# Kernel optimization log

Measured on AMD Instinct MI355X. Metric: run time of the kernel, lower is better.

## Reference

```python
import jax, jax.numpy as jnp
import numpy as np

OUT_FEATURES = 4096
IN_FEATURES = 16384
NNZ = 2_000_000
BATCH = 128


def setup_inputs() -> dict:
    key = jax.random.key(0)
    k1, k2, k3, k4, k5 = jax.random.split(key, 5)
    inputs = jax.random.normal(k1, (BATCH, IN_FEATURES), dtype=jnp.float32)
    # learned sparse weight values and bias (uniform init like reset_parameters)
    bound = 1.0 / (IN_FEATURES ** 0.5)
    values = jax.random.uniform(k2, (NNZ,), minval=-bound, maxval=bound, dtype=jnp.float32)
    bias = jax.random.uniform(k3, (OUT_FEATURES,), minval=-bound, maxval=bound, dtype=jnp.float32)
    # fixed COO connectivity: rows -> out_features, cols -> in_features
    rows = jax.random.randint(k4, (NNZ,), 0, OUT_FEATURES, dtype=jnp.int32)
    cols = jax.random.randint(k5, (NNZ,), 0, IN_FEATURES, dtype=jnp.int32)
    return {"inputs": inputs, "values": values, "bias": bias, "rows": rows, "cols": cols}


def reference(inputs, values, bias, rows, cols):
    # out[b, r] = sum_{k: rows[k]==r} values[k] * inputs[b, cols[k]]  (+ bias[r])
    # Gather input columns per nnz entry, scale, then scatter-add into output rows.
    contrib = inputs[:, cols] * values            # [B, nnz]
    out = jax.ops.segment_sum(contrib.T, rows, num_segments=OUT_FEATURES).T  # [B, out_features]
    return out + bias
```

## Files before the change

kernel.cpp:

```cpp
#include <hip/hip_runtime.h>
#include <hip/hip_fp16.h>

#define NNZ    2000000
#define BATCH  128
#define IN_F   16384
#define OUT_F  4096
#define NCH    512
#define CHUNK  ((NNZ + NCH - 1) / NCH)
#define NBK    1024
#define RPB    4
#define BK_CAP 2320

__device__ inline int mbcnt64(unsigned long long m) {
  return __builtin_amdgcn_mbcnt_hi((unsigned)(m >> 32),
         __builtin_amdgcn_mbcnt_lo((unsigned)m, 0));
}

__global__ __launch_bounds__(512)
void k_localsort(const int* __restrict__ rows, const int* __restrict__ cols,
                 const float* __restrict__ vals, int* __restrict__ desc,
                 int2* __restrict__ pairs) {
  __shared__ int  lrows[CHUNK];
  __shared__ int2 stage[CHUNK];
  __shared__ int  h[NBK], cur[NBK];
  __shared__ int  wsums[8];
  const int t = threadIdx.x, c = blockIdx.x;
  const int lane = t & 63, w = t >> 6;
  const int base = c * CHUNK;
  const int n = min(CHUNK, NNZ - base);

  h[t] = 0; h[t + 512] = 0;
  __syncthreads();
  for (int i = t; i < n; i += 512) {
    const int r = rows[base + i];
    lrows[i] = r;
    atomicAdd(&h[r >> 2], 1);
  }
  __syncthreads();
  const int v0 = h[2 * t], v1 = h[2 * t + 1];
  const int sv = v0 + v1;
  int x = sv;
#pragma unroll
  for (int off = 1; off < 64; off <<= 1) { int y = __shfl_up(x, off); if (lane >= off) x += y; }
  if (lane == 63) wsums[w] = x;
  __syncthreads();
  int wex = 0;
#pragma unroll
  for (int j = 0; j < 8; ++j) { const int sj = wsums[j]; wex += (j < w) ? sj : 0; }
  const int excl = wex + x - sv;
  cur[2 * t] = excl;
  cur[2 * t + 1] = excl + v0;
  ((int2*)desc)[c * 512 + t] = make_int2((excl << 8) | v0, ((excl + v0) << 8) | v1);
  __syncthreads();
  for (int i = t; i < n; i += 512) {
    const int r = lrows[i];
    const int pos = atomicAdd(&cur[r >> 2], 1);
    stage[pos] = make_int2((r << 14) | cols[base + i], __float_as_int(vals[base + i]));
  }
  __syncthreads();
  for (int j = t; j < n; j += 512) pairs[base + j] = stage[j];
}

__global__ __launch_bounds__(512)
void k_cscan(const int* __restrict__ desc, unsigned* __restrict__ rdesc,
             int* __restrict__ btot) {
  __shared__ int tile[16 * 513];
  const int t = threadIdx.x, blk = blockIdx.x;
  const int b0 = blk * 16;
  const int lane = t & 63, w = t >> 6;
#pragma unroll
  for (int it = 0; it < 16; ++it) {
    const int c = it * 32 + (t >> 4);
    tile[(t & 15) * 513 + c] = desc[c * NBK + b0 + (t & 15)];
  }
  __syncthreads();
#pragma unroll
  for (int k = 0; k < 2; ++k) {
    const int bl = 2 * w + k;
    int carry = 0;
#pragma unroll
    for (int j = 0; j < 8; ++j) {
      const int c = j * 64 + lane;
      const unsigned d = (unsigned)tile[bl * 513 + c];
      const int len = (int)(d & 255u);
      int x = len;
#pragma unroll
      for (int off = 1; off < 64; off <<= 1) { int y = __shfl_up(x, off); if (lane >= off) x += y; }
      const int ex = carry + x - len;
      rdesc[(b0 + bl) * NCH + c] = (d << 12) | (unsigned)ex;
      carry += __shfl(x, 63);
    }
    if (lane == 0) btot[b0 + bl] = carry;
  }
}

__global__ __launch_bounds__(256)
void k_transpose(const float* __restrict__ in, __half* __restrict__ inT) {
  __shared__ float tile[32][33];
  const int tx = threadIdx.x, ty = threadIdx.y;
  const int c0 = blockIdx.x * 32, b0 = blockIdx.y * 32;
#pragma unroll
  for (int j = 0; j < 32; j += 8)
    tile[ty + j][tx] = in[(b0 + ty + j) * IN_F + c0 + tx];
  __syncthreads();
#pragma unroll
  for (int j = 0; j < 32; j += 8)
    inT[(size_t)(c0 + ty + j) * BATCH + b0 + tx] = __float2half(tile[tx][ty + j]);
}

#define FMA8(V, X) do { \
    const __half2* hh = (const __half2*)&(X); \
    float2 f0 = __half22float2(hh[0]); \
    float2 f1 = __half22float2(hh[1]); \
    float2 f2 = __half22float2(hh[2]); \
    float2 f3 = __half22float2(hh[3]); \
    a0 = fmaf((V), f0.x, a0); a1 = fmaf((V), f0.y, a1); \
    a2 = fmaf((V), f1.x, a2); a3 = fmaf((V), f1.y, a3); \
    a4 = fmaf((V), f2.x, a4); a5 = fmaf((V), f2.y, a5); \
    a6 = fmaf((V), f3.x, a6); a7 = fmaf((V), f3.y, a7); \
  } while (0)

#define REFILL(SL, KK) do { \
    const int idx = (hh_ + 2 * (KK)) * 8 + 2 * g; \
    const int i0_ = (idx < nr) ? (s + idx) : 0; \
    const int i1_ = (idx + 1 < nr) ? (s + idx + 1) : 0; \
    const int2 p0 = sorted[i0_]; \
    const int2 p1 = sorted[i1_]; \
    v##SL##0 = (idx < nr) ? __int_as_float(p0.y) : 0.f; \
    v##SL##1 = (idx + 1 < nr) ? __int_as_float(p1.y) : 0.f; \
    x##SL##0 = inT[(p0.x & 16383) * 16 + q]; \
    x##SL##1 = inT[(p1.x & 16383) * 16 + q]; \
  } while (0)

#define STAGE(SL, NEXTKK) do { \
    FMA8(v##SL##0, x##SL##0); \
    FMA8(v##SL##1, x##SL##1); \
    REFILL(SL, NEXTKK); \
  } while (0)

__global__ __launch_bounds__(512, 8)
void k_spmm(const uint4* __restrict__ inT, const int2* __restrict__ pairs,
            const unsigned* __restrict__ rdesc, const int* __restrict__ btot,
            const float* __restrict__ bias, float* __restrict__ out) {
  __shared__ int2 staging[BK_CAP];
  __shared__ int2 sorted[BK_CAP];
  __shared__ int  exd[NCH];
  __shared__ float part[RPB][BATCH];
  __shared__ int  wrun[32];
  __shared__ unsigned long long wmask[32];
  __shared__ int  wcnt[32];
  __shared__ int  lst[RPB + 1];
  const int t = threadIdx.x, b = blockIdx.x;
  const int w = t >> 6, lane = t & 63;
  const int n = min(btot[b], BK_CAP);
  const int nrnd = (n + 511) & ~511;

  exd[t] = (int)rdesc[b * NCH + t];
  __syncthreads();
  for (int i = t; i < n; i += 512) {
    int lo = 0, hi = NCH - 1;
#pragma unroll
    for (int st = 0; st < 9; ++st) {
      const int mid = (lo + hi + 1) >> 1;
      if ((exd[mid] & 4095) <= i) lo = mid; else hi = mid - 1;
    }
    const unsigned d = (unsigned)exd[lo];
    staging[i] = pairs[lo * CHUNK + (int)(d >> 20) + (i - (int)(d & 4095u))];
  }
  __syncthreads();

  int cnt = 0;
  for (int i = w * 64 + lane; i < nrnd; i += 512) {
    const bool valid = i < n;
    const int key = valid ? staging[i].x : 0;
    const int r4 = valid ? ((key >> 14) & 3) : 4;
    unsigned long long m[4];
#pragma unroll
    for (int r = 0; r < 4; ++r) m[r] = __ballot(r4 == r);
    if (lane < 4) cnt += __popcll(m[lane]);
  }
  if (lane < 4) wcnt[w * 4 + lane] = cnt;
  __syncthreads();

  if (w == 0 && lane < 32) {
    const int v = wcnt[lane];
    int x = v;
#pragma unroll
    for (int off = 4; off < 32; off <<= 1) { int y = __shfl_up(x, off); if (lane >= off) x += y; }
    const int exw = x - v;
    int lstr = 0;
#pragma unroll
    for (int rr = 0; rr < 4; ++rr) {
      const int tr = __shfl(x, 28 + rr);
      if ((lane & 3) > rr) lstr += tr;
    }
    wrun[lane] = lstr + exw;
    if (lane < 4) lst[lane] = lstr;
    if (lane == 0) lst[RPB] = n;
  }
  __syncthreads();

  for (int i = w * 64 + lane; i < nrnd; i += 512) {
    const bool valid = i < n;
    const int2 p = valid ? staging[i] : make_int2(0, 0);
    const int r4 = valid ? ((p.x >> 14) & 3) : 4;
    unsigned long long m[4];
#pragma unroll
    for (int r = 0; r < 4; ++r) m[r] = __ballot(r4 == r);
    if (lane < 4) wmask[w * 4 + lane] = m[lane];
    if (valid) {
      const int rank = wrun[w * 4 + r4] + mbcnt64(wmask[w * 4 + r4]);
      sorted[rank] = p;
    }
    if (lane < 4) wrun[w * 4 + lane] += __popcll(m[lane]);
  }
  __syncthreads();

  const int rloc = w >> 1, hh_ = w & 1;
  const int r = b * RPB + rloc;
  const int g = lane >> 4, q = lane & 15;
  const int s = lst[rloc];
  const int nr = lst[rloc + 1] - s;
  const int nsteps = (nr + 7) >> 3;
  const int K = (nsteps + 1) >> 1;
  const int K3 = ((K + 2) / 3) * 3;

  float a0 = 0.f, a1 = 0.f, a2 = 0.f, a3 = 0.f, a4 = 0.f, a5 = 0.f, a6 = 0.f, a7 = 0.f;
  uint4 xA0, xA1, xB0, xB1, xC0, xC1;
  float vA0, vA1, vB0, vB1, vC0, vC1;

  REFILL(A, 0);
  REFILL(B, 1);
  REFILL(C, 2);
  for (int kk = 0; kk < K3; kk += 3) {
    STAGE(A, kk + 3);
    STAGE(B, kk + 4);
    STAGE(C, kk + 5);
  }

  a0 += __shfl_xor(a0, 16); a0 += __shfl_xor(a0, 32);
  a1 += __shfl_xor(a1, 16); a1 += __shfl_xor(a1, 32);
  a2 += __shfl_xor(a2, 16); a2 += __shfl_xor(a2, 32);
  a3 += __shfl_xor(a3, 16); a3 += __shfl_xor(a3, 32);
  a4 += __shfl_xor(a4, 16); a4 += __shfl_xor(a4, 32);
  a5 += __shfl_xor(a5, 16); a5 += __shfl_xor(a5, 32);
  a6 += __shfl_xor(a6, 16); a6 += __shfl_xor(a6, 32);
  a7 += __shfl_xor(a7, 16); a7 += __shfl_xor(a7, 32);

  if (hh_ == 1 && g == 0) {
    const int o = q * 8;
    part[rloc][o + 0] = a0; part[rloc][o + 1] = a1;
    part[rloc][o + 2] = a2; part[rloc][o + 3] = a3;
    part[rloc][o + 4] = a4; part[rloc][o + 5] = a5;
    part[rloc][o + 6] = a6; part[rloc][o + 7] = a7;
  }
  __syncthreads();
  if (hh_ == 0 && g == 0) {
    const float bs_ = bias[r];
    const int o = q * 8;
    out[(o + 0) * OUT_F + r] = a0 + part[rloc][o + 0] + bs_;
    out[(o + 1) * OUT_F + r] = a1 + part[rloc][o + 1] + bs_;
    out[(o + 2) * OUT_F + r] = a2 + part[rloc][o + 2] + bs_;
    out[(o + 3) * OUT_F + r] = a3 + part[rloc][o + 3] + bs_;
    out[(o + 4) * OUT_F + r] = a4 + part[rloc][o + 4] + bs_;
    out[(o + 5) * OUT_F + r] = a5 + part[rloc][o + 5] + bs_;
    out[(o + 6) * OUT_F + r] = a6 + part[rloc][o + 6] + bs_;
    out[(o + 7) * OUT_F + r] = a7 + part[rloc][o + 7] + bs_;
  }
}

extern "C" void kernel_launch(void* const* d_in, const int* in_sizes, int n_in,
                              void* d_out, int out_size, void* d_ws, size_t ws_size,
                              hipStream_t stream) {
  const float* inputs = (const float*)d_in[0];
  const float* values = (const float*)d_in[1];
  const float* bias   = (const float*)d_in[2];
  const int*   rows   = (const int*)d_in[3];
  const int*   cols   = (const int*)d_in[4];
  float* out = (float*)d_out;

  char* ws = (char*)d_ws;
  __half*   inputT = (__half*)(ws);
  int2*     pairs  = (int2*)(ws + 4194304);
  int*      desc   = (int*)(ws + 20194304);
  unsigned* rdesc  = (unsigned*)(ws + 22291456);
  int*      btot   = (int*)(ws + 24388608);

  k_localsort<<<NCH,      512, 0, stream>>>(rows, cols, values, desc, pairs);
  k_cscan    <<<NBK / 16, 512, 0, stream>>>(desc, rdesc, btot);
  k_transpose<<<dim3(IN_F / 32, BATCH / 32), dim3(32, 8), 0, stream>>>(inputs, inputT);
  k_spmm     <<<NBK,      512, 0, stream>>>((const uint4*)inputT, pairs, rdesc, btot, bias, out);
}
```

Measured before the change: 139.4 us.

## Use packed fp16 FMA accumulation, paired nnz loads, and finer local-sort chunks

The SpMM inner loop now accumulates with packed half2 FMAs into fp16 partial sums, flushed into fp32 accumulators every three stages. This replaces per-element half-to-float conversions and scalar fp32 FMAs. Each row segment in the sorted list is padded to even length so two nnz entries can be fetched with one 16-byte LDS load. The local sort uses 1024 chunks with int4/float4 vectorized loads and int4 stores, the column scan is retuned to match, and the reduction buffer reuses the staging shared memory to cut LDS footprint. Accumulating in fp16 reduces precision of the partial sums.

Result: faster. 133.2 us (-4.4%).

```diff
diff --git a/kernel.cpp b/kernel.cpp
--- a/kernel.cpp
+++ b/kernel.cpp
@@ -5,11 +5,11 @@
 #define BATCH  128
 #define IN_F   16384
 #define OUT_F  4096
-#define NCH    512
-#define CHUNK  ((NNZ + NCH - 1) / NCH)
+#define NCH    1024
+#define CHUNK  1956
 #define NBK    1024
 #define RPB    4
-#define BK_CAP 2320
+#define BK_CAP 2240
 
 __device__ inline int mbcnt64(unsigned long long m) {
   return __builtin_amdgcn_mbcnt_hi((unsigned)(m >> 32),
@@ -28,13 +28,17 @@
   const int lane = t & 63, w = t >> 6;
   const int base = c * CHUNK;
   const int n = min(CHUNK, NNZ - base);
+  const int n4 = n >> 2;
 
   h[t] = 0; h[t + 512] = 0;
   __syncthreads();
-  for (int i = t; i < n; i += 512) {
-    const int r = rows[base + i];
-    lrows[i] = r;
-    atomicAdd(&h[r >> 2], 1);
+  for (int i = t; i < n4; i += 512) {
+    const int4 r4 = ((const int4*)(rows + base))[i];
+    ((int4*)lrows)[i] = r4;
+    atomicAdd(&h[r4.x >> 2], 1);
+    atomicAdd(&h[r4.y >> 2], 1);
+    atomicAdd(&h[r4.z >> 2], 1);
+    atomicAdd(&h[r4.w >> 2], 1);
   }
   __syncthreads();
   const int v0 = h[2 * t], v1 = h[2 * t + 1];
@@ -52,46 +56,49 @@
   cur[2 * t + 1] = excl + v0;
   ((int2*)desc)[c * 512 + t] = make_int2((excl << 8) | v0, ((excl + v0) << 8) | v1);
   __syncthreads();
-  for (int i = t; i < n; i += 512) {
-    const int r = lrows[i];
-    const int pos = atomicAdd(&cur[r >> 2], 1);
-    stage[pos] = make_int2((r << 14) | cols[base + i], __float_as_int(vals[base + i]));
-  }
-  __syncthreads();
-  for (int j = t; j < n; j += 512) pairs[base + j] = stage[j];
+  for (int i = t; i < n4; i += 512) {
+    const int4   r4 = ((const int4*)lrows)[i];
+    const int4   c4 = ((const int4*)(cols + base))[i];
+    const float4 f4 = ((const float4*)(vals + base))[i];
+    int pos;
+    pos = atomicAdd(&cur[r4.x >> 2], 1); stage[pos] = make_int2((r4.x << 14) | c4.x, __float_as_int(f4.x));
+    pos = atomicAdd(&cur[r4.y >> 2], 1); stage[pos] = make_int2((r4.y << 14) | c4.y, __float_as_int(f4.y));
+    pos = atomicAdd(&cur[r4.z >> 2], 1); stage[pos] = make_int2((r4.z << 14) | c4.z, __float_as_int(f4.z));
+    pos = atomicAdd(&cur[r4.w >> 2], 1); stage[pos] = make_int2((r4.w << 14) | c4.w, __float_as_int(f4.w));
+  }
+  __syncthreads();
+  const int nh = n >> 1;
+  for (int j = t; j < nh; j += 512)
+    ((int4*)(pairs + base))[j] = ((const int4*)stage)[j];
 }
 
 __global__ __launch_bounds__(512)
 void k_cscan(const int* __restrict__ desc, unsigned* __restrict__ rdesc,
              int* __restrict__ btot) {
-  __shared__ int tile[16 * 513];
+  __shared__ int tile[8 * 1025];
   const int t = threadIdx.x, blk = blockIdx.x;
-  const int b0 = blk * 16;
+  const int b0 = blk * 8;
   const int lane = t & 63, w = t >> 6;
 #pragma unroll
   for (int it = 0; it < 16; ++it) {
-    const int c = it * 32 + (t >> 4);
-    tile[(t & 15) * 513 + c] = desc[c * NBK + b0 + (t & 15)];
-  }
-  __syncthreads();
-#pragma unroll
-  for (int k = 0; k < 2; ++k) {
-    const int bl = 2 * w + k;
-    int carry = 0;
-#pragma unroll
-    for (int j = 0; j < 8; ++j) {
-      const int c = j * 64 + lane;
-      const unsigned d = (unsigned)tile[bl * 513 + c];
-      const int len = (int)(d & 255u);
-      int x = len;
-#pragma unroll
-      for (int off = 1; off < 64; off <<= 1) { int y = __shfl_up(x, off); if (lane >= off) x += y; }
-      const int ex = carry + x - len;
-      rdesc[(b0 + bl) * NCH + c] = (d << 12) | (unsigned)ex;
-      carry += __shfl(x, 63);
-    }
-    if (lane == 0) btot[b0 + bl] = carry;
-  }
+    const int cc = it * 64 + (t >> 3);
+    tile[(t & 7) * 1025 + cc] = desc[cc * NBK + b0 + (t & 7)];
+  }
+  __syncthreads();
+  int carry = 0;
+#pragma unroll
+  for (int j = 0; j < 16; ++j) {
+    const int cc = j * 64 + lane;
+    const unsigned d = (unsigned)tile[w * 1025 + cc];
+    const int len = (int)(d & 255u);
+    int x = len;
+#pragma unroll
+    for (int off = 1; off < 64; off <<= 1) { int y = __shfl_up(x, off); if (lane >= off) x += y; }
+    const int ex = carry + x - len;
+    rdesc[(b0 + w) * NCH + cc] = (d << 12) | (unsigned)ex;
+    carry += __shfl(x, 63);
+  }
+  if (lane == 0) btot[b0 + w] = carry;
 }
 
 __global__ __launch_bounds__(256)
@@ -108,44 +115,45 @@
     inT[(size_t)(c0 + ty + j) * BATCH + b0 + tx] = __float2half(tile[tx][ty + j]);
 }
 
-#define FMA8(V, X) do { \
-    const __half2* hh = (const __half2*)&(X); \
-    float2 f0 = __half22float2(hh[0]); \
-    float2 f1 = __half22float2(hh[1]); \
-    float2 f2 = __half22float2(hh[2]); \
-    float2 f3 = __half22float2(hh[3]); \
-    a0 = fmaf((V), f0.x, a0); a1 = fmaf((V), f0.y, a1); \
-    a2 = fmaf((V), f1.x, a2); a3 = fmaf((V), f1.y, a3); \
-    a4 = fmaf((V), f2.x, a4); a5 = fmaf((V), f2.y, a5); \
-    a6 = fmaf((V), f3.x, a6); a7 = fmaf((V), f3.y, a7); \
-  } while (0)
-
 #define REFILL(SL, KK) do { \
     const int idx = (hh_ + 2 * (KK)) * 8 + 2 * g; \
-    const int i0_ = (idx < nr) ? (s + idx) : 0; \
-    const int i1_ = (idx + 1 < nr) ? (s + idx + 1) : 0; \
-    const int2 p0 = sorted[i0_]; \
-    const int2 p1 = sorted[i1_]; \
-    v##SL##0 = (idx < nr) ? __int_as_float(p0.y) : 0.f; \
-    v##SL##1 = (idx + 1 < nr) ? __int_as_float(p1.y) : 0.f; \
-    x##SL##0 = inT[(p0.x & 16383) * 16 + q]; \
-    x##SL##1 = inT[(p1.x & 16383) * 16 + q]; \
+    const bool vld = idx < nr; \
+    const int i0_ = vld ? (s + idx) : 0; \
+    uint4 pp = *((const uint4*)(sorted + i0_)); \
+    if (!vld) { pp.y = 0u; pp.w = 0u; } \
+    x##SL##0 = inT[(pp.x & 16383u) * 16 + q]; \
+    x##SL##1 = inT[(pp.z & 16383u) * 16 + q]; \
+    pv##SL = make_uint2(pp.y, pp.w); \
   } while (0)
 
-#define STAGE(SL, NEXTKK) do { \
-    FMA8(v##SL##0, x##SL##0); \
-    FMA8(v##SL##1, x##SL##1); \
-    REFILL(SL, NEXTKK); \
+#define FMAH(SL) do { \
+    const __half2 hv0 = __float2half2_rn(__uint_as_float(pv##SL.x)); \
+    const __half2 hv1 = __float2half2_rn(__uint_as_float(pv##SL.y)); \
+    const __half2* h0 = (const __half2*)&x##SL##0; \
+    const __half2* h1 = (const __half2*)&x##SL##1; \
+    hac0 = __hfma2(hv0, h0[0], hac0); hac1 = __hfma2(hv0, h0[1], hac1); \
+    hac2 = __hfma2(hv0, h0[2], hac2); hac3 = __hfma2(hv0, h0[3], hac3); \
+    hac0 = __hfma2(hv1, h1[0], hac0); hac1 = __hfma2(hv1, h1[1], hac1); \
+    hac2 = __hfma2(hv1, h1[2], hac2); hac3 = __hfma2(hv1, h1[3], hac3); \
+  } while (0)
+
+#define STAGE(SL, NEXTKK) do { FMAH(SL); REFILL(SL, NEXTKK); } while (0)
+
+#define FLUSH() do { \
+    float2 f0 = __half22float2(hac0), f1 = __half22float2(hac1); \
+    float2 f2 = __half22float2(hac2), f3 = __half22float2(hac3); \
+    a0 += f0.x; a1 += f0.y; a2 += f1.x; a3 += f1.y; \
+    a4 += f2.x; a5 += f2.y; a6 += f3.x; a7 += f3.y; \
+    hac0 = hz; hac1 = hz; hac2 = hz; hac3 = hz; \
   } while (0)
 
 __global__ __launch_bounds__(512, 8)
 void k_spmm(const uint4* __restrict__ inT, const int2* __restrict__ pairs,
             const unsigned* __restrict__ rdesc, const int* __restrict__ btot,
             const float* __restrict__ bias, float* __restrict__ out) {
-  __shared__ int2 staging[BK_CAP];
-  __shared__ int2 sorted[BK_CAP];
+  __shared__ __align__(16) int2 staging[BK_CAP];
+  __shared__ __align__(16) int2 sorted[BK_CAP + 8];
   __shared__ int  exd[NCH];
-  __shared__ float part[RPB][BATCH];
   __shared__ int  wrun[32];
   __shared__ unsigned long long wmask[32];
   __shared__ int  wcnt[32];
@@ -156,11 +164,12 @@
   const int nrnd = (n + 511) & ~511;
 
   exd[t] = (int)rdesc[b * NCH + t];
+  exd[t + 512] = (int)rdesc[b * NCH + t + 512];
   __syncthreads();
   for (int i = t; i < n; i += 512) {
     int lo = 0, hi = NCH - 1;
 #pragma unroll
-    for (int st = 0; st < 9; ++st) {
+    for (int st = 0; st < 10; ++st) {
       const int mid = (lo + hi + 1) >> 1;
       if ((exd[mid] & 4095) <= i) lo = mid; else hi = mid - 1;
     }
@@ -188,15 +197,20 @@
 #pragma unroll
     for (int off = 4; off < 32; off <<= 1) { int y = __shfl_up(x, off); if (lane >= off) x += y; }
     const int exw = x - v;
-    int lstr = 0;
+    int lstr = 0, tpad = 0;
 #pragma unroll
     for (int rr = 0; rr < 4; ++rr) {
       const int tr = __shfl(x, 28 + rr);
-      if ((lane & 3) > rr) lstr += tr;
+      const int trE = (tr + 1) & ~1;
+      if ((lane & 3) > rr) lstr += trE;
+      tpad += trE;
     }
     wrun[lane] = lstr + exw;
     if (lane < 4) lst[lane] = lstr;
-    if (lane == 0) lst[RPB] = n;
+    if (lane == 0) lst[RPB] = tpad;
+    if (lane >= 28) {
+      if (x & 1) sorted[lstr + x] = make_int2(0, 0);
+    }
   }
   __syncthreads();
 
@@ -226,8 +240,10 @@
   const int K3 = ((K + 2) / 3) * 3;
 
   float a0 = 0.f, a1 = 0.f, a2 = 0.f, a3 = 0.f, a4 = 0.f, a5 = 0.f, a6 = 0.f, a7 = 0.f;
+  const __half2 hz = __float2half2_rn(0.f);
+  __half2 hac0 = hz, hac1 = hz, hac2 = hz, hac3 = hz;
   uint4 xA0, xA1, xB0, xB1, xC0, xC1;
-  float vA0, vA1, vB0, vB1, vC0, vC1;
+  uint2 pvA, pvB, pvC;
 
   REFILL(A, 0);
   REFILL(B, 1);
@@ -236,6 +252,7 @@
     STAGE(A, kk + 3);
     STAGE(B, kk + 4);
     STAGE(C, kk + 5);
+    FLUSH();
   }
 
   a0 += __shfl_xor(a0, 16); a0 += __shfl_xor(a0, 32);
@@ -247,6 +264,7 @@
   a6 += __shfl_xor(a6, 16); a6 += __shfl_xor(a6, 32);
   a7 += __shfl_xor(a7, 16); a7 += __shfl_xor(a7, 32);
 
+  float (*part)[BATCH] = (float (*)[BATCH])staging;
   if (hh_ == 1 && g == 0) {
     const int o = q * 8;
     part[rloc][o + 0] = a0; part[rloc][o + 1] = a1;
@@ -282,12 +300,12 @@
   char* ws = (char*)d_ws;
   __half*   inputT = (__half*)(ws);
   int2*     pairs  = (int2*)(ws + 4194304);
-  int*      desc   = (int*)(ws + 20194304);
-  unsigned* rdesc  = (unsigned*)(ws + 22291456);
-  int*      btot   = (int*)(ws + 24388608);
-
-  k_localsort<<<NCH,      512, 0, stream>>>(rows, cols, values, desc, pairs);
-  k_cscan    <<<NBK / 16, 512, 0, stream>>>(desc, rdesc, btot);
+  int*      desc   = (int*)(ws + 20217856);
+  unsigned* rdesc  = (unsigned*)(ws + 24412160);
+  int*      btot   = (int*)(ws + 28606464);
+
+  k_localsort<<<NCH,     512, 0, stream>>>(rows, cols, values, desc, pairs);
+  k_cscan    <<<NBK / 8, 512, 0, stream>>>(desc, rdesc, btot);
   k_transpose<<<dim3(IN_F / 32, BATCH / 32), dim3(32, 8), 0, stream>>>(inputs, inputT);
-  k_spmm     <<<NBK,      512, 0, stream>>>((const uint4*)inputT, pairs, rdesc, btot, bias, out);
-}
+  k_spmm     <<<NBK,     512, 0, stream>>>((const uint4*)inputT, pairs, rdesc, btot, bias, out);
+}
```
